# Kernel tuning notes

Measured on AMD Instinct MI355X. Metric: run time of the kernel, lower is better.

The kernel has to match this reference:

```python
import jax, jax.numpy as jnp
import numpy as np

N_EMB = 1024
HEAD_SIZE = 128


def setup_inputs() -> dict:
    key = jax.random.key(0)
    k1, k2, k3, k4 = jax.random.split(key, 4)
    B, T = 8, 4096
    x = jax.random.normal(k1, (B, T, N_EMB), dtype=jnp.float32)
    # nn.Linear(n_emb, head_size, bias=False) weights have shape [head_size, n_emb]
    s = 1.0 / np.sqrt(N_EMB)
    Wq = jax.random.uniform(k2, (HEAD_SIZE, N_EMB), jnp.float32, -s, s)
    Wk = jax.random.uniform(k3, (HEAD_SIZE, N_EMB), jnp.float32, -s, s)
    Wv = jax.random.uniform(k4, (HEAD_SIZE, N_EMB), jnp.float32, -s, s)
    return {"x": x, "Wq": Wq, "Wk": Wk, "Wv": Wv}


def reference(x, Wq, Wk, Wv):
    # x: [B, T, C]; W*: [H, C]
    B, T, C = x.shape
    H = Wq.shape[0]
    q = jnp.einsum('btc,hc->bth', x, Wq)
    k = jnp.einsum('btc,hc->bth', x, Wk)
    v = jnp.einsum('btc,hc->bth', x, Wv)
    scale = H ** -0.5
    wei = jnp.einsum('bth,bsh->bts', q, k) * scale  # [B, T, T]
    # causal mask: position t attends to s <= t
    causal = jnp.arange(T)[:, None] >= jnp.arange(T)[None, :]
    wei = jnp.where(causal, wei, -jnp.inf)
    wei = jax.nn.softmax(wei, axis=-1)
    # dropout treated as identity (eval mode)
    out = jnp.einsum('bts,bsh->bth', wei, v)  # [B, T, H]
    return out
```

## Files before the change

### kernel.cpp

```cpp
#include <hip/hip_runtime.h>
#include <hip/hip_bf16.h>

typedef __bf16 bf16_t;
typedef __attribute__((ext_vector_type(8))) __bf16 bf16x8;
typedef __attribute__((ext_vector_type(4))) __bf16 bf16x4;
typedef __attribute__((ext_vector_type(4))) float f32x4;

#define MFMA16(a, b, c) __builtin_amdgcn_mfma_f32_16x16x32_bf16((a), (b), (c), 0, 0, 0)

__device__ __forceinline__ void gload_lds16(const void* g, void* l) {
    __builtin_amdgcn_global_load_lds(
        (const __attribute__((address_space(1))) void*)g,
        (__attribute__((address_space(3))) void*)l, 16, 0, 0);
}

__global__ __launch_bounds__(256, 3) void proj_qkv(
    const float* __restrict__ X,
    const float* __restrict__ W0, const float* __restrict__ W1, const float* __restrict__ W2,
    bf16_t* __restrict__ O0, bf16_t* __restrict__ O1, bf16_t* __restrict__ O2)
{
    __shared__ __align__(16) char As[128 * 128];
    __shared__ __align__(16) char Bs[128 * 128];

    const int tid = threadIdx.x;
    const int wid = tid >> 6;
    const int lane = tid & 63;
    const int l15 = lane & 15, l4 = lane >> 4;
    const int wr = wid >> 1, wc = wid & 1;
    const int m0 = blockIdx.x * 128;

    const float* W = (blockIdx.y == 0) ? W0 : (blockIdx.y == 1 ? W1 : W2);

    const int r0 = tid >> 4;
    const int kq = tid & 15;
    const int swz = ((r0 & 7) << 4);

    f32x4 acc[4][4] = {};
    float4 xr[8];

    #pragma unroll
    for (int i = 0; i < 8; ++i)
        xr[i] = *(const float4*)(X + (size_t)(m0 + r0 + i * 16) * 1024 + kq * 4);

    for (int ks = 0; ks < 16; ++ks) {
        const int kb = ks * 64;
        #pragma unroll
        for (int i = 0; i < 8; ++i) {
            const int r = r0 + i * 16;
            bf16x4 av; av[0] = (bf16_t)xr[i].x; av[1] = (bf16_t)xr[i].y;
            av[2] = (bf16_t)xr[i].z; av[3] = (bf16_t)xr[i].w;
            *(bf16x4*)(As + r * 128 + ((kq * 8) ^ swz)) = av;
        }
        #pragma unroll
        for (int i = 0; i < 8; ++i) {
            const int r = r0 + i * 16;
            float4 wa = *(const float4*)(W + (size_t)r * 1024 + kb + kq * 4);
            bf16x4 wv; wv[0] = (bf16_t)wa.x; wv[1] = (bf16_t)wa.y;
            wv[2] = (bf16_t)wa.z; wv[3] = (bf16_t)wa.w;
            *(bf16x4*)(Bs + r * 128 + ((kq * 8) ^ swz)) = wv;
        }
        __syncthreads();
        if (ks < 15) {
            #pragma unroll
            for (int i = 0; i < 8; ++i)
                xr[i] = *(const float4*)(X + (size_t)(m0 + r0 + i * 16) * 1024 + kb + 64 + kq * 4);
        }
        #pragma unroll
        for (int kk = 0; kk < 64; kk += 32) {
            const int kbyte = 2 * kk + 16 * l4;
            bf16x8 af[4], bfr[4];
            #pragma unroll
            for (int mi = 0; mi < 4; ++mi) {
                int r = wr * 64 + mi * 16 + l15;
                af[mi] = *(const bf16x8*)(As + r * 128 + (kbyte ^ ((r & 7) << 4)));
            }
            #pragma unroll
            for (int ni = 0; ni < 4; ++ni) {
                int r = wc * 64 + ni * 16 + l15;
                bfr[ni] = *(const bf16x8*)(Bs + r * 128 + (kbyte ^ ((r & 7) << 4)));
            }
            #pragma unroll
            for (int mi = 0; mi < 4; ++mi)
                #pragma unroll
                for (int ni = 0; ni < 4; ++ni)
                    acc[mi][ni] = MFMA16(af[mi], bfr[ni], acc[mi][ni]);
        }
        __syncthreads();
    }

    if (blockIdx.y < 2) {
        const float sc = (blockIdx.y == 0) ? 0.12751754816f : 1.0f;
        bf16_t* O = (blockIdx.y == 0) ? O0 : O1;
        #pragma unroll
        for (int mi = 0; mi < 4; ++mi)
            #pragma unroll
            for (int ni = 0; ni < 4; ++ni) {
                int row = m0 + wr * 64 + mi * 16 + l4 * 4;
                int col = wc * 64 + ni * 16 + l15;
                #pragma unroll
                for (int r = 0; r < 4; ++r)
                    O[(size_t)(row + r) * 128 + col] = (bf16_t)(acc[mi][ni][r] * sc);
            }
    } else {
        #pragma unroll
        for (int mi = 0; mi < 4; ++mi)
            #pragma unroll
            for (int ni = 0; ni < 4; ++ni) {
                int row0 = m0 + wr * 64 + mi * 16 + l4 * 4;
                int col = wc * 64 + ni * 16 + l15;
                int bb = row0 >> 12, t0 = row0 & 4095;
                bf16x4 pk;
                #pragma unroll
                for (int r = 0; r < 4; ++r) pk[r] = (bf16_t)acc[mi][ni][r];
                *(bf16x4*)(O2 + ((size_t)bb << 19) + (size_t)col * 4096 + t0) = pk;
            }
    }
}

__global__ __launch_bounds__(256, 2) void attn_fwd(
    const bf16_t* __restrict__ Qb, const bf16_t* __restrict__ Kb,
    const bf16_t* __restrict__ Vtg, float* __restrict__ out, int Bn)
{
    __shared__ __align__(16) char lds[73728];

    const int tid = threadIdx.x, wid = tid >> 6, lane = tid & 63;
    const int l15 = lane & 15, l4 = lane >> 4;

    const int blk = blockIdx.x;
    const int b = blk % Bn;
    const int j = blk / Bn;

    const size_t base = (size_t)b * 4096 * 128;
    const size_t baseVT = (size_t)b << 19;

    char* Vw = lds + wid * 16384;
    char* Pw = lds + 65536 + wid * 2048;

    const int sh = lane >> 2;
    const int skb = (lane & 3) * 8;

    for (int seg = 0; seg < 2; ++seg) {
        const int p = seg ? (127 - j) : j;
        const int q0 = p << 5;
        const int nt = (p >= wid) ? ((p - wid) >> 2) + 1 : 0;

        bf16x8 aq[2][4];
        #pragma unroll
        for (int qs = 0; qs < 2; ++qs)
            #pragma unroll
            for (int kf = 0; kf < 4; ++kf)
                aq[qs][kf] = *(const bf16x8*)(Qb + base
                    + (size_t)(q0 + 16 * qs + l15) * 128 + 32 * kf + 8 * l4);

        float mx[2] = {-1e30f, -1e30f}, lsum[2] = {0.f, 0.f};
        f32x4 o[2][8] = {};
        bf16x8 kreg[2][4];

        auto stageV = [&](int i) {
            const int kv0 = (wid + 4 * i) << 5;
            char* dst = Vw + (i & 1) * 8192;
            #pragma unroll
            for (int c = 0; c < 8; ++c) {
                const bf16_t* src = Vtg + baseVT + (size_t)(16 * c + sh) * 4096 + kv0 + skb;
                gload_lds16(src, dst + c * 1024);
            }
        };
        auto loadK = [&](int i) {
            const int kv0 = (wid + 4 * i) << 5;
            const bf16_t* kp = Kb + base + (size_t)(kv0 + l15) * 128 + 8 * l4;
            #pragma unroll
            for (int ni = 0; ni < 2; ++ni)
                #pragma unroll
                for (int kf = 0; kf < 4; ++kf)
                    kreg[ni][kf] = *(const bf16x8*)(kp + (size_t)ni * 2048 + kf * 32);
        };

        if (nt > 0) { loadK(0); stageV(0); }

        for (int i = 0; i < nt; ++i) {
            const int lt = wid + 4 * i;
            const int kv0 = lt << 5;

            f32x4 sa[2][2];
            #pragma unroll
            for (int qs = 0; qs < 2; ++qs)
                #pragma unroll
                for (int ni = 0; ni < 2; ++ni) sa[qs][ni] = (f32x4){0.f, 0.f, 0.f, 0.f};
            __builtin_amdgcn_s_setprio(1);
            #pragma unroll
            for (int kf = 0; kf < 4; ++kf)
                #pragma unroll
                for (int ni = 0; ni < 2; ++ni) {
                    sa[0][ni] = MFMA16(kreg[ni][kf], aq[0][kf], sa[0][ni]);
                    sa[1][ni] = MFMA16(kreg[ni][kf], aq[1][kf], sa[1][ni]);
                }
            __builtin_amdgcn_s_setprio(0);

            if (i + 1 < nt) loadK(i + 1);

            if (lt == p) {
                #pragma unroll
                for (int qs = 0; qs < 2; ++qs) {
                    const int qg = q0 + 16 * qs + l15;
                    #pragma unroll
                    for (int ni = 0; ni < 2; ++ni)
                        #pragma unroll
                        for (int r = 0; r < 4; ++r)
                            if (kv0 + 16 * ni + 4 * l4 + r > qg) sa[qs][ni][r] = -1e30f;
                }
            }

            #pragma unroll
            for (int qs = 0; qs < 2; ++qs) {
                float tm = sa[qs][0][0];
                #pragma unroll
                for (int ni = 0; ni < 2; ++ni)
                    #pragma unroll
                    for (int r = 0; r < 4; ++r) tm = fmaxf(tm, sa[qs][ni][r]);
                tm = fmaxf(tm, __shfl_xor(tm, 16, 64));
                tm = fmaxf(tm, __shfl_xor(tm, 32, 64));
                if (__any(tm > mx[qs])) {
                    const float mnew = fmaxf(mx[qs], tm);
                    const float c = exp2f(mx[qs] - mnew);
                    lsum[qs] *= c;
                    #pragma unroll
                    for (int mf = 0; mf < 8; ++mf) {
                        f32x4 t = o[qs][mf];
                        t[0] *= c; t[1] *= c; t[2] *= c; t[3] *= c;
                        o[qs][mf] = t;
                    }
                    mx[qs] = mnew;
                }
                float ss = 0.f;
                #pragma unroll
                for (int ni = 0; ni < 2; ++ni)
                    #pragma unroll
                    for (int r = 0; r < 4; ++r) {
                        float pv = exp2f(sa[qs][ni][r] - mx[qs]);
                        sa[qs][ni][r] = pv;
                        ss += pv;
                    }
                ss += __shfl_xor(ss, 16, 64);
                ss += __shfl_xor(ss, 32, 64);
                lsum[qs] += ss;
                #pragma unroll
                for (int ni = 0; ni < 2; ++ni) {
                    bf16x4 pv;
                    pv[0] = (bf16_t)sa[qs][ni][0]; pv[1] = (bf16_t)sa[qs][ni][1];
                    pv[2] = (bf16_t)sa[qs][ni][2]; pv[3] = (bf16_t)sa[qs][ni][3];
                    *(bf16x4*)(Pw + (16 * qs + l15) * 64 + 32 * ni + 8 * l4) = pv;
                }
            }

            __builtin_amdgcn_sched_barrier(0);
            asm volatile("s_waitcnt vmcnt(8)" ::: "memory");
            __builtin_amdgcn_sched_barrier(0);

            char* Vbuf = Vw + (i & 1) * 8192;
            bf16x8 pa0 = *(const bf16x8*)(Pw + l15 * 64 + 16 * l4);
            bf16x8 pa1 = *(const bf16x8*)(Pw + (16 + l15) * 64 + 16 * l4);
            __builtin_amdgcn_s_setprio(1);
            #pragma unroll
            for (int mf = 0; mf < 8; ++mf) {
                bf16x8 av = *(const bf16x8*)(Vbuf + (16 * mf + l15) * 64 + 16 * l4);
                o[0][mf] = MFMA16(av, pa0, o[0][mf]);
                o[1][mf] = MFMA16(av, pa1, o[1][mf]);
            }
            __builtin_amdgcn_s_setprio(0);

            if (i + 1 < nt) stageV(i + 1);
        }

        asm volatile("s_waitcnt vmcnt(0)" ::: "memory");
        __syncthreads();
        #pragma unroll
        for (int qs = 0; qs < 2; ++qs)
            #pragma unroll
            for (int mf = 0; mf < 8; ++mf)
                *(f32x4*)(lds + wid * 16384 + (qs * 8 + mf) * 1024 + lane * 16) = o[qs][mf];
        if (l4 == 0) {
            #pragma unroll
            for (int qs = 0; qs < 2; ++qs)
                *(float2*)(lds + 65536 + wid * 256 + (qs * 16 + l15) * 8)
                    = make_float2(mx[qs], lsum[qs]);
        }
        __syncthreads();
        #pragma unroll
        for (int qs = 0; qs < 2; ++qs) {
            float mw[4], lw[4];
            #pragma unroll
            for (int w = 0; w < 4; ++w) {
                float2 st = *(const float2*)(lds + 65536 + w * 256 + (qs * 16 + l15) * 8);
                mw[w] = st.x; lw[w] = st.y;
            }
            const float M = fmaxf(fmaxf(mw[0], mw[1]), fmaxf(mw[2], mw[3]));
            float cw[4], L = 0.f;
            #pragma unroll
            for (int w = 0; w < 4; ++w) { cw[w] = exp2f(mw[w] - M); L += lw[w] * cw[w]; }
            const float inv = 1.f / L;
            #pragma unroll
            for (int mm = 0; mm < 2; ++mm) {
                const int mf = 2 * wid + mm;
                f32x4 acc = (f32x4){0.f, 0.f, 0.f, 0.f};
                #pragma unroll
                for (int w = 0; w < 4; ++w) {
                    f32x4 v = *(const f32x4*)(lds + w * 16384 + (qs * 8 + mf) * 1024 + lane * 16);
                    #pragma unroll
                    for (int e = 0; e < 4; ++e) acc[e] += v[e] * cw[w];
                }
                #pragma unroll
                for (int e = 0; e < 4; ++e) acc[e] *= inv;
                float* op = out + ((size_t)b * 4096 + q0 + 16 * qs + l15) * 128 + 16 * mf + 4 * l4;
                *(f32x4*)op = acc;
            }
        }
        __syncthreads();
    }
}

extern "C" void kernel_launch(void* const* d_in, const int* in_sizes, int n_in,
                              void* d_out, int out_size, void* d_ws, size_t ws_size,
                              hipStream_t stream) {
    const float* X  = (const float*)d_in[0];
    const float* Wq = (const float*)d_in[1];
    const float* Wk = (const float*)d_in[2];
    const float* Wv = (const float*)d_in[3];
    float* out = (float*)d_out;

    const int M = in_sizes[0] / 1024;
    const int Bn = M / 4096;

    bf16_t* Qb  = (bf16_t*)d_ws;
    bf16_t* KbP = Qb + (size_t)M * 128;
    bf16_t* VtP = KbP + (size_t)M * 128;

    proj_qkv<<<dim3(M / 128, 3), 256, 0, stream>>>(X, Wq, Wk, Wv, Qb, KbP, VtP);
    attn_fwd<<<dim3(64 * Bn), 256, 0, stream>>>(Qb, KbP, VtP, out, Bn);
}
```

Measured before the change: 139.7 us.

## Load V tiles directly into registers instead of staging through LDS

Drops the global-to-LDS double-buffered staging of the transposed V tiles. Each lane now loads its V fragments straight into registers and prefetches the next tile after the PV MFMAs. The P scratch writes and reads in LDS also get an XOR swizzle to reduce bank conflicts. This removes the LDS round trip and the manual vmcnt wait, but raises register pressure and the V global loads are strided 16-byte rows.

```diff
diff --git a/kernel.cpp b/kernel.cpp
--- a/kernel.cpp
+++ b/kernel.cpp
@@ -7,12 +7,6 @@
 typedef __attribute__((ext_vector_type(4))) float f32x4;
 
 #define MFMA16(a, b, c) __builtin_amdgcn_mfma_f32_16x16x32_bf16((a), (b), (c), 0, 0, 0)
-
-__device__ __forceinline__ void gload_lds16(const void* g, void* l) {
-    __builtin_amdgcn_global_load_lds(
-        (const __attribute__((address_space(1))) void*)g,
-        (__attribute__((address_space(3))) void*)l, 16, 0, 0);
-}
 
 __global__ __launch_bounds__(256, 3) void proj_qkv(
     const float* __restrict__ X,
@@ -133,11 +127,8 @@
     const size_t base = (size_t)b * 4096 * 128;
     const size_t baseVT = (size_t)b << 19;
 
-    char* Vw = lds + wid * 16384;
     char* Pw = lds + 65536 + wid * 2048;
-
-    const int sh = lane >> 2;
-    const int skb = (lane & 3) * 8;
+    const int pswz = (l15 >> 1) & 3;
 
     for (int seg = 0; seg < 2; ++seg) {
         const int p = seg ? (127 - j) : j;
@@ -155,16 +146,8 @@
         float mx[2] = {-1e30f, -1e30f}, lsum[2] = {0.f, 0.f};
         f32x4 o[2][8] = {};
         bf16x8 kreg[2][4];
-
-        auto stageV = [&](int i) {
-            const int kv0 = (wid + 4 * i) << 5;
-            char* dst = Vw + (i & 1) * 8192;
-            #pragma unroll
-            for (int c = 0; c < 8; ++c) {
-                const bf16_t* src = Vtg + baseVT + (size_t)(16 * c + sh) * 4096 + kv0 + skb;
-                gload_lds16(src, dst + c * 1024);
-            }
-        };
+        bf16x8 vreg[8];
+
         auto loadK = [&](int i) {
             const int kv0 = (wid + 4 * i) << 5;
             const bf16_t* kp = Kb + base + (size_t)(kv0 + l15) * 128 + 8 * l4;
@@ -174,8 +157,15 @@
                 for (int kf = 0; kf < 4; ++kf)
                     kreg[ni][kf] = *(const bf16x8*)(kp + (size_t)ni * 2048 + kf * 32);
         };
-
-        if (nt > 0) { loadK(0); stageV(0); }
+        auto loadV = [&](int i) {
+            const int kv0 = (wid + 4 * i) << 5;
+            const bf16_t* vp = Vtg + baseVT + (size_t)l15 * 4096 + kv0 + 8 * l4;
+            #pragma unroll
+            for (int mf = 0; mf < 8; ++mf)
+                vreg[mf] = *(const bf16x8*)(vp + (size_t)(16 * mf) * 4096);
+        };
+
+        if (nt > 0) { loadK(0); loadV(0); }
 
         for (int i = 0; i < nt; ++i) {
             const int lt = wid + 4 * i;
@@ -248,30 +238,24 @@
                     bf16x4 pv;
                     pv[0] = (bf16_t)sa[qs][ni][0]; pv[1] = (bf16_t)sa[qs][ni][1];
                     pv[2] = (bf16_t)sa[qs][ni][2]; pv[3] = (bf16_t)sa[qs][ni][3];
-                    *(bf16x4*)(Pw + (16 * qs + l15) * 64 + 32 * ni + 8 * l4) = pv;
-                }
-            }
-
-            __builtin_amdgcn_sched_barrier(0);
-            asm volatile("s_waitcnt vmcnt(8)" ::: "memory");
-            __builtin_amdgcn_sched_barrier(0);
-
-            char* Vbuf = Vw + (i & 1) * 8192;
-            bf16x8 pa0 = *(const bf16x8*)(Pw + l15 * 64 + 16 * l4);
-            bf16x8 pa1 = *(const bf16x8*)(Pw + (16 + l15) * 64 + 16 * l4);
+                    *(bf16x4*)(Pw + (16 * qs + l15) * 64
+                               + (((2 * ni + (l4 >> 1)) ^ pswz) << 4) + 8 * (l4 & 1)) = pv;
+                }
+            }
+
+            bf16x8 pa0 = *(const bf16x8*)(Pw + l15 * 64 + ((l4 ^ pswz) << 4));
+            bf16x8 pa1 = *(const bf16x8*)(Pw + (16 + l15) * 64 + ((l4 ^ pswz) << 4));
             __builtin_amdgcn_s_setprio(1);
             #pragma unroll
             for (int mf = 0; mf < 8; ++mf) {
-                bf16x8 av = *(const bf16x8*)(Vbuf + (16 * mf + l15) * 64 + 16 * l4);
-                o[0][mf] = MFMA16(av, pa0, o[0][mf]);
-                o[1][mf] = MFMA16(av, pa1, o[1][mf]);
+                o[0][mf] = MFMA16(vreg[mf], pa0, o[0][mf]);
+                o[1][mf] = MFMA16(vreg[mf], pa1, o[1][mf]);
             }
             __builtin_amdgcn_s_setprio(0);
 
-            if (i + 1 < nt) stageV(i + 1);
-        }
-
-        asm volatile("s_waitcnt vmcnt(0)" ::: "memory");
+            if (i + 1 < nt) loadV(i + 1);
+        }
+
         __syncthreads();
         #pragma unroll
         for (int qs = 0; qs < 2; ++qs)
```

Measured after the change: 173.7 us. 24.3% more time.
